# Kernel tuning notes

Hardware: AMD Instinct MI355X
Metric: run time of the kernel (lower is better)

## Reference

```python
import jax, jax.numpy as jnp
import numpy as np

B, L, V, AV, D = 4, 512, 32128, 32000, 768
TAU = 1.0

def setup_inputs() -> dict:
    key = jax.random.key(0)
    k1, k2, k3, k4, k5 = jax.random.split(key, 5)
    logits = jax.random.normal(k1, (B, L, V), jnp.float32)
    gumbel_u = jax.random.uniform(k2, (B, L, V), jnp.float32, minval=1e-6, maxval=1.0 - 1e-6)
    word_embeddings = jax.random.normal(k3, (AV, D), jnp.float32) * 0.02
    # realistic prefix attention mask (ones then zero padding)
    lengths = jax.random.randint(k4, (B,), 128, L)
    rwrt_attention = (jnp.arange(L)[None, :] < lengths[:, None]).astype(jnp.int32)
    psg_input = jax.random.randint(k5, (B, L), 1, AV).astype(jnp.int32)
    return {"logits": logits, "gumbel_u": gumbel_u, "word_embeddings": word_embeddings,
            "rwrt_attention": rwrt_attention, "psg_input": psg_input}

def reference(logits, gumbel_u, word_embeddings, rwrt_attention, psg_input):
    # --- F.gumbel_softmax(logits, tau, hard=True) ---
    g = -jnp.log(-jnp.log(gumbel_u))                       # gumbel noise
    y_soft = jax.nn.softmax((logits + g) / TAU, axis=-1)    # [B,L,V]
    hard_idx = jnp.argmax(y_soft, axis=-1)                  # [B,L]
    y_hard = jax.nn.one_hot(hard_idx, V, dtype=logits.dtype)
    y = y_hard + y_soft - jax.lax.stop_gradient(y_soft)     # straight-through
    gumbel_output = y[..., :AV]                             # [B,L,AV]
    # --- the nested python loop is exactly a one-hot-weighted gather = GEMM ---
    inputs_embeds = jnp.einsum('blv,vd->bld', gumbel_output, word_embeddings)  # [B,L,D]
    mask = rwrt_attention.astype(logits.dtype)[..., None]
    inputs_embeds = inputs_embeds * mask
    # --- passage: torch.roll(psg,1,1); psg[:,0]=1 ---
    psg = jnp.roll(psg_input, 1, axis=1).at[:, 0].set(1)
    # flipped inverted mask selects padding region of flipped attention
    flipped_mask = 1 - jnp.fliplr(rwrt_attention)           # [B,L]
    extr_psg = flipped_mask * psg
    # roll_by_gather: roll each row right by its number of attended tokens
    shifts = jnp.sum(rwrt_attention == 1, axis=1)           # [B]
    pos = (jnp.arange(L)[None, :] - shifts[:, None]) % L    # [B,L]
    trunc_ids = jnp.take_along_axis(extr_psg, pos, axis=1)  # [B,L]
    # flag logic: leading idx==0 positions stay 0.0; once a nonzero id is seen,
    # every subsequent position (including id==0 -> pad embedding) is embedded
    flag = jnp.cumsum((trunc_ids != 0).astype(jnp.int32), axis=1) > 0  # [B,L]
    psg_embeds = jnp.where(flag[..., None], word_embeddings[trunc_ids], jnp.float32(0.0))
    return inputs_embeds + psg_embeds                        # [B,L,D]
```

## Files before the change

### kernel.cpp

```cpp
#include <hip/hip_runtime.h>
#include <hip/hip_bf16.h>
#include <math.h>

#define BB 4
#define LL 512
#define VV 32128
#define AVV 32000
#define DD 768
#define V4 (VV / 4)
#define D4 (DD / 4)

__device__ __forceinline__ float neg_log_u(float u) {
    float x = 1.0f - u;
    float q = 0.1f;
    q = fmaf(q, x, 1.0f / 9.0f);
    q = fmaf(q, x, 0.125f);
    q = fmaf(q, x, 1.0f / 7.0f);
    q = fmaf(q, x, 1.0f / 6.0f);
    q = fmaf(q, x, 0.2f);
    q = fmaf(q, x, 0.25f);
    q = fmaf(q, x, 1.0f / 3.0f);
    q = fmaf(q, x, 0.5f);
    float tpoly = fmaf(x * x, q, x);
    float tnat  = -__logf(u);
    return (u > 0.75f) ? tpoly : tnat;
}

__device__ __forceinline__ float gumbel_key(float lg, float u) {
    return lg - __logf(neg_log_u(u));
}

__global__ __launch_bounds__(256) void k_argmax(const float* __restrict__ logits,
                                                const float* __restrict__ gu,
                                                int* __restrict__ hidx) {
    const int row = blockIdx.x;
    const float4* lg4 = (const float4*)(logits + (size_t)row * VV);
    const float4* gu4 = (const float4*)(gu + (size_t)row * VV);

    float bkA = -INFINITY, bkB = -INFINITY;
    int   biA = 0, biB = 0;

    int i = threadIdx.x;
    for (; i + 256 < V4; i += 512) {
        float4 l0 = lg4[i];
        float4 u0 = gu4[i];
        float4 l1 = lg4[i + 256];
        float4 u1 = gu4[i + 256];

        float a0 = gumbel_key(l0.x, u0.x);
        float a1 = gumbel_key(l0.y, u0.y);
        float a2 = gumbel_key(l0.z, u0.z);
        float a3 = gumbel_key(l0.w, u0.w);
        float mA = fmaxf(fmaxf(a0, a1), fmaxf(a2, a3));
        if (mA > bkA) { bkA = mA; biA = i; }

        float b0 = gumbel_key(l1.x, u1.x);
        float b1 = gumbel_key(l1.y, u1.y);
        float b2 = gumbel_key(l1.z, u1.z);
        float b3 = gumbel_key(l1.w, u1.w);
        float mB = fmaxf(fmaxf(b0, b1), fmaxf(b2, b3));
        if (mB > bkB) { bkB = mB; biB = i + 256; }
    }
    if (i < V4) {
        float4 l0 = lg4[i];
        float4 u0 = gu4[i];
        float a0 = gumbel_key(l0.x, u0.x);
        float a1 = gumbel_key(l0.y, u0.y);
        float a2 = gumbel_key(l0.z, u0.z);
        float a3 = gumbel_key(l0.w, u0.w);
        float mA = fmaxf(fmaxf(a0, a1), fmaxf(a2, a3));
        if (mA > bkA) { bkA = mA; biA = i; }
    }

    float bk; int bi;
    if (bkB > bkA || (bkB == bkA && biB < biA)) { bk = bkB; bi = biB; }
    else                                        { bk = bkA; bi = biA; }

    {
        float4 lv = lg4[bi];
        float4 uv = gu4[bi];
        float k0 = gumbel_key(lv.x, uv.x);
        float k1 = gumbel_key(lv.y, uv.y);
        float k2 = gumbel_key(lv.z, uv.z);
        int j = (k0 == bk) ? 0 : ((k1 == bk) ? 1 : ((k2 == bk) ? 2 : 3));
        bi = bi * 4 + j;
    }

    for (int off = 32; off > 0; off >>= 1) {
        float ok = __shfl_down(bk, off);
        int   oi = __shfl_down(bi, off);
        if (ok > bk || (ok == bk && oi < bi)) { bk = ok; bi = oi; }
    }

    __shared__ float sk[4];
    __shared__ int   si[4];
    const int wid = threadIdx.x >> 6;
    if ((threadIdx.x & 63) == 0) { sk[wid] = bk; si[wid] = bi; }
    __syncthreads();
    if (threadIdx.x == 0) {
        for (int w = 1; w < 4; ++w) {
            if (sk[w] > bk || (sk[w] == bk && si[w] < bi)) { bk = sk[w]; bi = si[w]; }
        }
        hidx[row] = bi;
    }
}

__global__ __launch_bounds__(512) void k_tokens(const int* __restrict__ rwrt,
                                                const int* __restrict__ psg_in,
                                                const int* __restrict__ hidx,
                                                int2* __restrict__ toks) {
    __shared__ int s[LL];
    const int b = blockIdx.x;
    const int l = threadIdx.x;

    const int rw = rwrt[b * LL + l];

    s[l] = (rw == 1) ? 1 : 0;
    __syncthreads();
    for (int off = LL / 2; off > 0; off >>= 1) {
        if (l < off) s[l] += s[l + off];
        __syncthreads();
    }
    const int shifts = s[0];
    __syncthreads();

    const int pos = (l - shifts) & (LL - 1);
    const int psgv = (pos == 0) ? 1 : psg_in[b * LL + pos - 1];
    const int flip = 1 - rwrt[b * LL + (LL - 1 - pos)];
    const int trunc = flip * psgv;

    s[l] = (trunc != 0) ? 1 : 0;
    __syncthreads();
    for (int off = 1; off < LL; off <<= 1) {
        int v = (l >= off) ? s[l - off] : 0;
        __syncthreads();
        s[l] |= v;
        __syncthreads();
    }
    const int flag = s[l];

    const int h = hidx[b * LL + l];
    const int tokA = (rw != 0 && h < AVV) ? h : -1;
    const int tokP = flag ? trunc : -1;
    toks[b * LL + l] = make_int2(tokA, tokP);
}

__global__ __launch_bounds__(192) void k_out(const float* __restrict__ emb,
                                             const int2* __restrict__ toks,
                                             float* __restrict__ out) {
    const int row = blockIdx.x;
    const int t = threadIdx.x;
    const int2 tk = toks[row];

    float4 acc = make_float4(0.f, 0.f, 0.f, 0.f);
    if (tk.x >= 0) {
        float4 e = ((const float4*)(emb + (size_t)tk.x * DD))[t];
        acc.x += e.x; acc.y += e.y; acc.z += e.z; acc.w += e.w;
    }
    if (tk.y >= 0) {
        float4 e = ((const float4*)(emb + (size_t)tk.y * DD))[t];
        acc.x += e.x; acc.y += e.y; acc.z += e.z; acc.w += e.w;
    }
    ((float4*)out)[(size_t)row * D4 + t] = acc;
}

extern "C" void kernel_launch(void* const* d_in, const int* in_sizes, int n_in,
                              void* d_out, int out_size, void* d_ws, size_t ws_size,
                              hipStream_t stream) {
    const float* logits = (const float*)d_in[0];
    const float* gu     = (const float*)d_in[1];
    const float* emb    = (const float*)d_in[2];
    const int*   rwrt   = (const int*)d_in[3];
    const int*   psg    = (const int*)d_in[4];
    float* out = (float*)d_out;

    int*  hidx = (int*)d_ws;
    int2* toks = (int2*)((char*)d_ws + BB * LL * sizeof(int));

    k_argmax<<<BB * LL, 256, 0, stream>>>(logits, gu, hidx);
    k_tokens<<<BB, LL, 0, stream>>>(rwrt, psg, hidx, toks);
    k_out<<<BB * LL, 192, 0, stream>>>(emb, toks, out);
}
```

Before: 558.6 us.

## Prune gumbel argmax with cheap bit-trick upper bound and wave-level skip

Replaces the per-element exact gumbel key evaluation with a cheap upper bound computed from the integer bit pattern of (1-u). The exact log-based key is evaluated only when some lane in the wavefront could beat the current wave-wide best. The loop is also unrolled to four float4 loads per iteration. This cuts transcendental work in a kernel that is likely dominated by streaming logits and noise from memory. In exchange it adds ballot and shuffle overhead, and it relies on the bound constants being valid for correctness.

After: 554.7 us. Within noise of the previous version (-0.7%).

```diff
diff --git a/kernel.cpp b/kernel.cpp
--- a/kernel.cpp
+++ b/kernel.cpp
@@ -25,9 +25,32 @@
     float tnat  = -__logf(u);
     return (u > 0.75f) ? tpoly : tnat;
 }
-
 __device__ __forceinline__ float gumbel_key(float lg, float u) {
     return lg - __logf(neg_log_u(u));
+}
+
+#define UB_SCALE 8.2629583e-8f
+#define UB_C     88.0796919f
+__device__ __forceinline__ float ub_core(float lg, float u) {
+    float x = 1.0f - u;
+    float a = (float)__float_as_int(x);
+    return fmaf(a, -UB_SCALE, lg);
+}
+__device__ __forceinline__ float ub4(const float4& l, const float4& u) {
+    return fmaxf(fmaxf(ub_core(l.x, u.x), ub_core(l.y, u.y)),
+                 fmaxf(ub_core(l.z, u.z), ub_core(l.w, u.w)));
+}
+__device__ __forceinline__ void exact4(const float4& lv, const float4& uv, int base,
+                                       float& bk, int& bi) {
+    float k0 = gumbel_key(lv.x, uv.x);
+    float k1 = gumbel_key(lv.y, uv.y);
+    float k2 = gumbel_key(lv.z, uv.z);
+    float k3 = gumbel_key(lv.w, uv.w);
+    float m = fmaxf(fmaxf(k0, k1), fmaxf(k2, k3));
+    if (m > bk) {
+        int j = (k0 == m) ? 0 : ((k1 == m) ? 1 : ((k2 == m) ? 2 : 3));
+        bk = m; bi = base * 4 + j;
+    }
 }
 
 __global__ __launch_bounds__(256) void k_argmax(const float* __restrict__ logits,
@@ -37,53 +60,40 @@
     const float4* lg4 = (const float4*)(logits + (size_t)row * VV);
     const float4* gu4 = (const float4*)(gu + (size_t)row * VV);
 
-    float bkA = -INFINITY, bkB = -INFINITY;
-    int   biA = 0, biB = 0;
+    float bk = -INFINITY;
+    int   bi = 0;
+    float wbest = -INFINITY;
 
     int i = threadIdx.x;
-    for (; i + 256 < V4; i += 512) {
-        float4 l0 = lg4[i];
-        float4 u0 = gu4[i];
-        float4 l1 = lg4[i + 256];
-        float4 u1 = gu4[i + 256];
+    for (; i + 768 < V4; i += 1024) {
+        float4 l0 = lg4[i];       float4 u0 = gu4[i];
+        float4 l1 = lg4[i + 256]; float4 u1 = gu4[i + 256];
+        float4 l2 = lg4[i + 512]; float4 u2 = gu4[i + 512];
+        float4 l3 = lg4[i + 768]; float4 u3 = gu4[i + 768];
 
-        float a0 = gumbel_key(l0.x, u0.x);
-        float a1 = gumbel_key(l0.y, u0.y);
-        float a2 = gumbel_key(l0.z, u0.z);
-        float a3 = gumbel_key(l0.w, u0.w);
-        float mA = fmaxf(fmaxf(a0, a1), fmaxf(a2, a3));
-        if (mA > bkA) { bkA = mA; biA = i; }
-
-        float b0 = gumbel_key(l1.x, u1.x);
-        float b1 = gumbel_key(l1.y, u1.y);
-        float b2 = gumbel_key(l1.z, u1.z);
-        float b3 = gumbel_key(l1.w, u1.w);
-        float mB = fmaxf(fmaxf(b0, b1), fmaxf(b2, b3));
-        if (mB > bkB) { bkB = mB; biB = i + 256; }
+        float g = fmaxf(fmaxf(ub4(l0, u0), ub4(l1, u1)),
+                        fmaxf(ub4(l2, u2), ub4(l3, u3)));
+        if (__any(g > wbest - UB_C)) {
+            exact4(l0, u0, i,       bk, bi);
+            exact4(l1, u1, i + 256, bk, bi);
+            exact4(l2, u2, i + 512, bk, bi);
+            exact4(l3, u3, i + 768, bk, bi);
+            float m = bk;
+            for (int off = 32; off > 0; off >>= 1)
+                m = fmaxf(m, __shfl_xor(m, off));
+            wbest = m;
+        }
     }
-    if (i < V4) {
-        float4 l0 = lg4[i];
-        float4 u0 = gu4[i];
-        float a0 = gumbel_key(l0.x, u0.x);
-        float a1 = gumbel_key(l0.y, u0.y);
-        float a2 = gumbel_key(l0.z, u0.z);
-        float a3 = gumbel_key(l0.w, u0.w);
-        float mA = fmaxf(fmaxf(a0, a1), fmaxf(a2, a3));
-        if (mA > bkA) { bkA = mA; biA = i; }
-    }
-
-    float bk; int bi;
-    if (bkB > bkA || (bkB == bkA && biB < biA)) { bk = bkB; bi = biB; }
-    else                                        { bk = bkA; bi = biA; }
-
-    {
-        float4 lv = lg4[bi];
-        float4 uv = gu4[bi];
-        float k0 = gumbel_key(lv.x, uv.x);
-        float k1 = gumbel_key(lv.y, uv.y);
-        float k2 = gumbel_key(lv.z, uv.z);
-        int j = (k0 == bk) ? 0 : ((k1 == bk) ? 1 : ((k2 == bk) ? 2 : 3));
-        bi = bi * 4 + j;
+    for (; i < V4; i += 256) {
+        float4 l0 = lg4[i]; float4 u0 = gu4[i];
+        float g = ub4(l0, u0);
+        if (__any(g > wbest - UB_C)) {
+            exact4(l0, u0, i, bk, bi);
+            float m = bk;
+            for (int off = 32; off > 0; off >>= 1)
+                m = fmaxf(m, __shfl_xor(m, off));
+            wbest = m;
+        }
     }
 
     for (int off = 32; off > 0; off >>= 1) {
```
